# Kernel optimization log

Hardware: AMD Instinct MI355X
Metric: run time of the kernel (lower is better)

## Reference

```python
import jax, jax.numpy as jnp
import numpy as np

B, C, H, W = 8, 512, 64, 64
S = 64
STD = 0.001  # torch init.normal_(weight, std=0.001)


def setup_inputs() -> dict:
    key = jax.random.key(0)
    ks = jax.random.split(key, 7)
    return {
        "queries": jax.random.normal(ks[0], (B, C, H, W), dtype=jnp.float32),
        "k": jax.random.normal(ks[1], (B, C, H, W), dtype=jnp.float32),
        "v": jax.random.normal(ks[2], (B, C, H, W), dtype=jnp.float32),
        "Wq": jax.random.normal(ks[3], (S, C), dtype=jnp.float32) * STD,
        "Wk": jax.random.normal(ks[4], (S, C), dtype=jnp.float32) * STD,
        "Wv": jax.random.normal(ks[5], (S, C), dtype=jnp.float32) * STD,
        "Wl": jax.random.normal(ks[6], (C, S), dtype=jnp.float32) * STD,
    }


def _branch(A, Bp, Cp, Wl):
    # A,Bp,Cp: [h,w,b,S] projected tensors
    m = jnp.einsum('hwbs,hwbt->hwst', A, Bp)          # [h,w,S,S]
    m = jax.nn.softmax(m, axis=1)                      # softmax over w (dim=1, as in torch)
    o = jnp.einsum('hwst,hwbt->hwsb', m, Cp)           # [h,w,S,b]
    o = o / jnp.sum(o, axis=2, keepdims=True)          # normalize over S
    o = jnp.einsum('hwsb,cs->hwbc', o, Wl)             # transpose + Linear(S->C)
    return jnp.transpose(o, (2, 3, 0, 1))              # [b,c,h,w]


def reference(queries, k, v, Wq, Wk, Wv, Wl):
    q = jnp.transpose(queries, (2, 3, 0, 1))  # [h,w,b,c]
    kk = jnp.transpose(k, (2, 3, 0, 1))
    vv = jnp.transpose(v, (2, 3, 0, 1))
    aq = jnp.einsum('hwbc,sc->hwbs', q, Wq)   # [h,w,b,S]
    ak = jnp.einsum('hwbc,sc->hwbs', kk, Wk)
    av = jnp.einsum('hwbc,sc->hwbs', vv, Wv)
    out_q = _branch(aq, ak, av, Wl)
    out_k = _branch(ak, av, aq, Wl)
    out_v = _branch(av, aq, ak, Wl)
    return jnp.concatenate((out_q, out_k, out_v), axis=0)  # [3b,c,h,w]
```

## Files before the change

### kernel.cpp

```cpp
#include <hip/hip_runtime.h>
#include <hip/hip_bf16.h>

#define HW 4096
#define CCH 512
#define SDIM 64
#define BDIM 8

typedef __attribute__((ext_vector_type(8))) short short8;
typedef __attribute__((ext_vector_type(4))) float f32x4;

static __device__ __forceinline__ ushort f2bf(float f) {
  __hip_bfloat16 h = __float2bfloat16(f);
  return *reinterpret_cast<ushort*>(&h);
}
static __device__ __forceinline__ float bf2f(ushort u) {
  union { unsigned int u32; float f; } c;
  c.u32 = ((unsigned int)u) << 16;
  return c.f;
}
static __device__ __forceinline__ ushort trunc_bf(float f, float* rem) {
  union { float f; unsigned int u; } a; a.f = f;
  union { float f; unsigned int u; } h; h.u = a.u & 0xFFFF0000u;
  *rem = f - h.f;
  return (ushort)(a.u >> 16);
}
static __device__ __forceinline__ ushort rne_bf(float f) {
  union { float f; unsigned int u; } a; a.f = f;
  return (ushort)((a.u + 0x8000u) >> 16);
}
static __device__ __forceinline__ void gll16(const void* g, void* lds_base) {
  __builtin_amdgcn_global_load_lds(
      (const __attribute__((address_space(1))) unsigned int*)g,
      (__attribute__((address_space(3))) unsigned int*)lds_base, 16, 0, 0);
}

__global__ __launch_bounds__(256) void prep_kernel(const float* __restrict__ Wq,
                                                   const float* __restrict__ Wk,
                                                   const float* __restrict__ Wv,
                                                   const float* __restrict__ Wl,
                                                   ushort* __restrict__ whi,
                                                   ushort* __restrict__ wmid,
                                                   ushort* __restrict__ wlo,
                                                   ushort* __restrict__ wlhi,
                                                   ushort* __restrict__ wllo) {
  const int idx = blockIdx.x * 1024 + threadIdx.x * 4;
  if (blockIdx.y == 3) {
    float4 f = *reinterpret_cast<const float4*>(&Wl[idx]);
    ushort4 h, l;
    float r;
    h.x = trunc_bf(f.x, &r); l.x = rne_bf(r);
    h.y = trunc_bf(f.y, &r); l.y = rne_bf(r);
    h.z = trunc_bf(f.z, &r); l.z = rne_bf(r);
    h.w = trunc_bf(f.w, &r); l.w = rne_bf(r);
    *reinterpret_cast<ushort4*>(&wlhi[idx]) = h;
    *reinterpret_cast<ushort4*>(&wllo[idx]) = l;
    return;
  }
  const float* W = blockIdx.y == 0 ? Wq : (blockIdx.y == 1 ? Wk : Wv);
  float4 f = *reinterpret_cast<const float4*>(&W[idx]);
  ushort4 h, m, l;
  float r, r2;
  h.x = f2bf(f.x); r = f.x - bf2f(h.x); m.x = f2bf(r); r2 = r - bf2f(m.x); l.x = f2bf(r2);
  h.y = f2bf(f.y); r = f.y - bf2f(h.y); m.y = f2bf(r); r2 = r - bf2f(m.y); l.y = f2bf(r2);
  h.z = f2bf(f.z); r = f.z - bf2f(h.z); m.z = f2bf(r); r2 = r - bf2f(m.z); l.z = f2bf(r2);
  h.w = f2bf(f.w); r = f.w - bf2f(h.w); m.w = f2bf(r); r2 = r - bf2f(m.w); l.w = f2bf(r2);
  const size_t o = (size_t)blockIdx.y * (SDIM * CCH) + idx;
  *reinterpret_cast<ushort4*>(&whi[o])  = h;
  *reinterpret_cast<ushort4*>(&wmid[o]) = m;
  *reinterpret_cast<ushort4*>(&wlo[o])  = l;
}

__global__ __launch_bounds__(256) void proj_mfma_kernel(const float* __restrict__ q,
                                                        const float* __restrict__ k,
                                                        const float* __restrict__ v,
                                                        const ushort* __restrict__ whi,
                                                        const ushort* __restrict__ wmid,
                                                        const ushort* __restrict__ wlo,
                                                        float* __restrict__ ap) {
  __shared__ float Xs[2][32 * 128];
  __shared__ ushort Ws[2][3][64 * 32];
  const int mt = blockIdx.x;
  const int b = blockIdx.y;
  const int br = blockIdx.z;
  const float* x = br == 0 ? q : (br == 1 ? k : v);
  const ushort* wsrc[3] = {whi + (size_t)br * SDIM * CCH,
                           wmid + (size_t)br * SDIM * CCH,
                           wlo + (size_t)br * SDIM * CCH};
  float* apo = ap + (size_t)br * HW * 512;
  const int hw0 = mt * 128;
  const int tid = threadIdx.x;
  const int l = tid & 63;
  const int wid = tid >> 6;
  const int wstrip = wid * 32;
  const int row16 = l & 15;
  const int kgrp = l >> 4;
  const float* xcol = x + (size_t)b * CCH * HW + hw0;
  const int rbase = 8 * wid;
  const int rsub = l >> 5;
  const int wrow = wid * 16 + (l >> 2);
  const int wblk = (l & 3) ^ ((l >> 3) & 3);
  const int jp = kgrp ^ ((row16 >> 1) & 3);
  const int xswz = (kgrp & 1) << 4;

  f32x4 acc_hi[2][4] = {};
  f32x4 acc_co[2][4] = {};

#define STAGE(BUF, CI)                                                            \
  do {                                                                            \
    _Pragma("unroll") for (int j = 0; j < 4; ++j) {                               \
      const int r = rbase + 2 * j + rsub;                                         \
      const int hwsrc = (((l & 31) ^ ((((r) >> 3) & 1) << 2)) * 4);               \
      gll16(xcol + (size_t)((CI) * 32 + r) * HW + hwsrc,                          \
            &Xs[BUF][(rbase + 2 * j) * 128]);                                     \
    }                                                                             \
    _Pragma("unroll") for (int lv = 0; lv < 3; ++lv)                              \
      gll16(wsrc[lv] + (size_t)wrow * CCH + (CI) * 32 + wblk * 8,                 \
            &Ws[BUF][lv][wid * 512]);                                             \
  } while (0)

  STAGE(0, 0);

  for (int ci = 0; ci < 16; ++ci) {
    __builtin_amdgcn_sched_barrier(0);
    if (ci < 15) {
      STAGE((ci + 1) & 1, ci + 1);
      __builtin_amdgcn_sched_barrier(0);
      asm volatile("s_waitcnt vmcnt(7)" ::: "memory");
    } else {
      asm volatile("s_waitcnt vmcnt(0)" ::: "memory");
    }
    __builtin_amdgcn_sched_barrier(0);
    __builtin_amdgcn_s_barrier();
    __builtin_amdgcn_sched_barrier(0);

    short8 bh[4], bm[4], bl[4];
#pragma unroll
    for (int nf = 0; nf < 4; ++nf) {
      const int woff = (nf * 16 + row16) * 32 + jp * 8;
      bh[nf] = *reinterpret_cast<const short8*>(&Ws[ci & 1][0][woff]);
      bm[nf] = *reinterpret_cast<const short8*>(&Ws[ci & 1][1][woff]);
      bl[nf] = *reinterpret_cast<const short8*>(&Ws[ci & 1][2][woff]);
    }

    const float* lw = &Xs[ci & 1][0];
#pragma unroll
    for (int mf = 0; mf < 2; ++mf) {
      const int rowA = (wstrip + mf * 16 + row16) ^ xswz;
      short8 ah, am, al;
      {
        ushort th[8], tm[8], tl[8];
#pragma unroll
        for (int i = 0; i < 8; ++i) {
          const float f = lw[(kgrp * 8 + i) * 128 + rowA];
          float r, r2;
          th[i] = trunc_bf(f, &r);
          tm[i] = trunc_bf(r, &r2);
          tl[i] = rne_bf(r2);
        }
        ah = *reinterpret_cast<const short8*>(th);
        am = *reinterpret_cast<const short8*>(tm);
        al = *reinterpret_cast<const short8*>(tl);
      }
#pragma unroll
      for (int nf = 0; nf < 4; ++nf) {
        acc_hi[mf][nf] = __builtin_amdgcn_mfma_f32_16x16x32_bf16(ah, bh[nf], acc_hi[mf][nf], 0, 0, 0);
        acc_co[mf][nf] = __builtin_amdgcn_mfma_f32_16x16x32_bf16(ah, bm[nf], acc_co[mf][nf], 0, 0, 0);
        acc_co[mf][nf] = __builtin_amdgcn_mfma_f32_16x16x32_bf16(am, bh[nf], acc_co[mf][nf], 0, 0, 0);
        acc_co[mf][nf] = __builtin_amdgcn_mfma_f32_16x16x32_bf16(am, bm[nf], acc_co[mf][nf], 0, 0, 0);
        acc_co[mf][nf] = __builtin_amdgcn_mfma_f32_16x16x32_bf16(ah, bl[nf], acc_co[mf][nf], 0, 0, 0);
        acc_co[mf][nf] = __builtin_amdgcn_mfma_f32_16x16x32_bf16(al, bh[nf], acc_co[mf][nf], 0, 0, 0);
        acc_co[mf][nf] = __builtin_amdgcn_mfma_f32_16x16x32_bf16(am, bl[nf], acc_co[mf][nf], 0, 0, 0);
        acc_co[mf][nf] = __builtin_amdgcn_mfma_f32_16x16x32_bf16(al, bm[nf], acc_co[mf][nf], 0, 0, 0);
      }
    }
    __builtin_amdgcn_sched_barrier(0);
    __builtin_amdgcn_s_barrier();
    __builtin_amdgcn_sched_barrier(0);
  }
#undef STAGE

#pragma unroll
  for (int mf = 0; mf < 2; ++mf)
#pragma unroll
    for (int nf = 0; nf < 4; ++nf)
#pragma unroll
      for (int r = 0; r < 4; ++r) {
        const int m = hw0 + wstrip + mf * 16 + kgrp * 4 + r;
        apo[(size_t)m * 512 + b * 64 + nf * 16 + row16] = acc_hi[mf][nf][r] + acc_co[mf][nf][r];
      }
}

__global__ __launch_bounds__(512) void denom_kernel(const float* __restrict__ ap,
                                                    float* __restrict__ rD) {
  __shared__ float As[3][128];
  __shared__ float Bs[3][512];
  const int h = blockIdx.x, br = blockIdx.y, sq = blockIdx.z;
  const float* A  = ap + ((size_t)br * HW + (size_t)h * 64) * 512;
  const float* Bp = ap + ((size_t)((br + 1) % 3) * HW + (size_t)h * 64) * 512;
  const int tid = threadIdx.x;
  const int t = tid & 63;
  const int sg = tid >> 6;
  float D[2] = {};

#define STAGE_D(BUF, W)                                                        \
  do {                                                                         \
    if (sg == 0) {                                                             \
      if (t < 32)                                                              \
        gll16(A + (size_t)(W) * 512 + (t >> 2) * 64 + sq * 16 + (t & 3) * 4,   \
              &As[BUF][0]);                                                    \
    } else if (sg == 1) {                                                      \
      gll16(Bp + (size_t)(W) * 512 + t * 4, &Bs[BUF][0]);                      \
    } else if (sg == 2) {                                                      \
      gll16(Bp + (size_t)(W) * 512 + 256 + t * 4, &Bs[BUF][256]);              \
    }                                                                          \
  } while (0)

  STAGE_D(0, 0);

  for (int w = 0; w < 64; ++w) {
    __builtin_amdgcn_sched_barrier(0);
    if (w < 63) {
      STAGE_D((w + 1) % 3, w + 1);
      __builtin_amdgcn_sched_barrier(0);
      asm volatile("s_waitcnt vmcnt(1)" ::: "memory");
    } else {
      asm volatile("s_waitcnt vmcnt(0)" ::: "memory");
    }
    __builtin_amdgcn_sched_barrier(0);
    __builtin_amdgcn_s_barrier();
    __builtin_amdgcn_sched_barrier(0);

    const float* Aw = &As[w % 3][0];
    const float* Bw = &Bs[w % 3][0];
    float bv[8];
#pragma unroll
    for (int b = 0; b < 8; ++b) bv[b] = Bw[b * 64 + t];
#pragma unroll
    for (int j = 0; j < 2; ++j) {
      const int sl = sg * 2 + j;
      float m = 0.f;
#pragma unroll
      for (int b = 0; b < 8; ++b) m = fmaf(Aw[b * 16 + sl], bv[b], m);
      D[j] += __expf(m);
    }
  }
#undef STAGE_D

#pragma unroll
  for (int j = 0; j < 2; ++j)
    rD[((size_t)(br * 64 + h) * 64 + sq * 16 + sg * 2 + j) * 64 + t] = 1.0f / D[j];
}

__global__ __launch_bounds__(256) void attn_kernel(const float* __restrict__ ap,
                                                   const float* __restrict__ rD,
                                                   float* __restrict__ on) {
  __shared__ float Tile[3][3 * 512];
  __shared__ float Ms[64 * 68];
  const int wc = blockIdx.x, h = blockIdx.y, br = blockIdx.z;
  const float* A  = ap + ((size_t)br * HW + h * 64) * 512;
  const float* Bp = ap + ((size_t)((br + 1) % 3) * HW + h * 64) * 512;
  const float* Cp = ap + ((size_t)((br + 2) % 3) * HW + h * 64) * 512;
  const float* rDp = rD + (size_t)(br * 64 + h) * 4096;
  const int tid = threadIdx.x;
  const int t = tid & 63;
  const int sg = tid >> 6;
  const int w0 = wc * 8;

  float rdv[16];
#pragma unroll
  for (int j = 0; j < 16; ++j) rdv[j] = rDp[(sg * 16 + j) * 64 + t];

  const float* src = sg == 0 ? A : (sg == 1 ? Bp : Cp);

#define STAGE_T(BUF, W)                                                   \
  do {                                                                    \
    if (sg < 3) {                                                         \
      _Pragma("unroll") for (int j = 0; j < 2; ++j)                       \
        gll16(src + (size_t)(W) * 512 + j * 256 + t * 4,                  \
              &Tile[BUF][sg * 512 + j * 256]);                            \
    }                                                                     \
  } while (0)

  STAGE_T(0, w0);

  for (int wi = 0; wi < 8; ++wi) {
    __builtin_amdgcn_sched_barrier(0);
    if (wi < 7) {
      STAGE_T((wi + 1) % 3, w0 + wi + 1);
      __builtin_amdgcn_sched_barrier(0);
      asm volatile("s_waitcnt vmcnt(2)" ::: "memory");
    } else {
      asm volatile("s_waitcnt vmcnt(0)" ::: "memory");
    }
    __builtin_amdgcn_sched_barrier(0);
    asm volatile("s_waitcnt lgkmcnt(0)" ::: "memory");
    __builtin_amdgcn_s_barrier();
    __builtin_amdgcn_sched_barrier(0);

    const float* Aw = &Tile[wi % 3][0];
    const float* Bw = &Tile[wi % 3][512];
    const float* Cw = &Tile[wi % 3][1024];
    {
      float bv[8];
#pragma unroll
      for (int b = 0; b < 8; ++b) bv[b] = Bw[b * 64 + t];
#pragma unroll
      for (int j4 = 0; j4 < 4; ++j4) {
        const int s0 = sg * 16 + j4 * 4;
        float4 ma = make_float4(0.f, 0.f, 0.f, 0.f);
#pragma unroll
        for (int b = 0; b < 8; ++b) {
          const float4 av = *reinterpret_cast<const float4*>(&Aw[b * 64 + s0]);
          ma.x = fmaf(av.x, bv[b], ma.x);
          ma.y = fmaf(av.y, bv[b], ma.y);
          ma.z = fmaf(av.z, bv[b], ma.z);
          ma.w = fmaf(av.w, bv[b], ma.w);
        }
        Ms[(s0 + 0) * 68 + t] = __expf(ma.x) * rdv[j4 * 4 + 0];
        Ms[(s0 + 1) * 68 + t] = __expf(ma.y) * rdv[j4 * 4 + 1];
        Ms[(s0 + 2) * 68 + t] = __expf(ma.z) * rdv[j4 * 4 + 2];
        Ms[(s0 + 3) * 68 + t] = __expf(ma.w) * rdv[j4 * 4 + 3];
      }
    }
    __builtin_amdgcn_sched_barrier(0);
    asm volatile("s_waitcnt lgkmcnt(0)" ::: "memory");
    __builtin_amdgcn_s_barrier();
    __builtin_amdgcn_sched_barrier(0);

    float o0 = 0.f, o1 = 0.f;
#pragma unroll
    for (int tt = 0; tt < 64; tt += 4) {
      const float4 mv = *reinterpret_cast<const float4*>(&Ms[t * 68 + tt]);
      const float4 c0 = *reinterpret_cast<const float4*>(&Cw[sg * 64 + tt]);
      const float4 c1 = *reinterpret_cast<const float4*>(&Cw[(sg + 4) * 64 + tt]);
      o0 = fmaf(mv.w, c0.w, fmaf(mv.z, c0.z, fmaf(mv.y, c0.y, fmaf(mv.x, c0.x, o0))));
      o1 = fmaf(mv.w, c1.w, fmaf(mv.z, c1.z, fmaf(mv.y, c1.y, fmaf(mv.x, c1.x, o1))));
    }
    float n0 = o0, n1 = o1;
#pragma unroll
    for (int off = 32; off > 0; off >>= 1) {
      n0 += __shfl_xor(n0, off);
      n1 += __shfl_xor(n1, off);
    }
    const float r0 = 1.0f / n0, r1 = 1.0f / n1;
    const size_t ob = ((size_t)br * HW + h * 64 + w0 + wi) * 512;
    on[ob + (size_t)sg * 64 + t] = o0 * r0;
    on[ob + (size_t)(sg + 4) * 64 + t] = o1 * r1;
  }
#undef STAGE_T
}

__global__ __launch_bounds__(256) void out_kernel(const float* __restrict__ on,
                                                  const ushort* __restrict__ wlhi,
                                                  const ushort* __restrict__ wllo,
                                                  float* __restrict__ out) {
  __shared__ float Os[128 * 68];
  const int hwt = blockIdx.x;
  const int brb = blockIdx.y;
  const int br = brb >> 3, b = brb & 7;
  const int hw0 = hwt * 128;
  const int tid = threadIdx.x;
  const int l = tid & 63;
  const int wv = tid >> 6;
  const int l15 = l & 15;
  const int kgrp = l >> 4;

  {
    const int row = tid >> 4;
    const int s4 = (tid & 15) * 4;
#pragma unroll
    for (int it = 0; it < 8; ++it) {
      const int r = row + it * 16;
      *reinterpret_cast<float4*>(&Os[r * 68 + s4]) =
          *reinterpret_cast<const float4*>(&on[((size_t)(br * HW + hw0 + r) * 8 + b) * 64 + s4]);
    }
  }
  __syncthreads();

  short8 onh[2][2], onl[2][2];
#pragma unroll
  for (int nf = 0; nf < 2; ++nf)
#pragma unroll
    for (int ks = 0; ks < 2; ++ks) {
      const int row = wv * 32 + nf * 16 + l15;
      const float* p = &Os[row * 68 + ks * 32 + kgrp * 8];
      ushort th[8], tl[8];
#pragma unroll
      for (int i = 0; i < 8; ++i) {
        float r;
        th[i] = trunc_bf(p[i], &r);
        tl[i] = rne_bf(r);
      }
      onh[nf][ks] = *reinterpret_cast<const short8*>(th);
      onl[nf][ks] = *reinterpret_cast<const short8*>(tl);
    }

  for (int mf = 0; mf < 32; ++mf) {
    f32x4 acc[2] = {};
#pragma unroll
    for (int ks = 0; ks < 2; ++ks) {
      const size_t woff = (size_t)(mf * 16 + l15) * 64 + ks * 32 + kgrp * 8;
      const short8 wh8 = *reinterpret_cast<const short8*>(&wlhi[woff]);
      const short8 wl8 = *reinterpret_cast<const short8*>(&wllo[woff]);
#pragma unroll
      for (int nf = 0; nf < 2; ++nf) {
        acc[nf] = __builtin_amdgcn_mfma_f32_16x16x32_bf16(wh8, onh[nf][ks], acc[nf], 0, 0, 0);
        acc[nf] = __builtin_amdgcn_mfma_f32_16x16x32_bf16(wh8, onl[nf][ks], acc[nf], 0, 0, 0);
        acc[nf] = __builtin_amdgcn_mfma_f32_16x16x32_bf16(wl8, onh[nf][ks], acc[nf], 0, 0, 0);
      }
    }
#pragma unroll
    for (int nf = 0; nf < 2; ++nf)
#pragma unroll
      for (int r = 0; r < 4; ++r) {
        const int cc = mf * 16 + kgrp * 4 + r;
        out[(size_t)(brb * 512 + cc) * HW + hw0 + wv * 32 + nf * 16 + l15] = acc[nf][r];
      }
  }
}

extern "C" void kernel_launch(void* const* d_in, const int* in_sizes, int n_in,
                              void* d_out, int out_size, void* d_ws, size_t ws_size,
                              hipStream_t stream) {
  const float* q  = (const float*)d_in[0];
  const float* k  = (const float*)d_in[1];
  const float* v  = (const float*)d_in[2];
  const float* Wq = (const float*)d_in[3];
  const float* Wk = (const float*)d_in[4];
  const float* Wv = (const float*)d_in[5];
  const float* Wl = (const float*)d_in[6];
  float* out = (float*)d_out;

  float* ap = (float*)d_ws;
  float* rD = ap + (size_t)3 * HW * 512;
  float* on = rD + (size_t)3 * 64 * 64 * 64;
  ushort* whi  = (ushort*)rD;
  ushort* wmid = whi + (size_t)3 * SDIM * CCH;
  ushort* wlo  = wmid + (size_t)3 * SDIM * CCH;
  ushort* wlhi = (ushort*)(on + (size_t)3 * HW * 512);
  ushort* wllo = wlhi + (size_t)SDIM * CCH;

  prep_kernel<<<dim3(32, 4), 256, 0, stream>>>(Wq, Wk, Wv, Wl, whi, wmid, wlo, wlhi, wllo);
  proj_mfma_kernel<<<dim3(32, 8, 3), 256, 0, stream>>>(q, k, v, whi, wmid, wlo, ap);
  denom_kernel<<<dim3(64, 3, 4), 512, 0, stream>>>(ap, rD);
  attn_kernel<<<dim3(8, 64, 3), 256, 0, stream>>>(ap, rD, on);
  out_kernel<<<dim3(32, 24), 256, 0, stream>>>(on, wlhi, wllo, out);
}
```

Measured before the change: 234.7 us.

## Software-pipeline attn_kernel: overlap PV of previous column with QK of next

Double-buffers the Ms score tile in shared memory so that each iteration computes the PV product for column wi-1 and the QK/exp scores for column wi between a single barrier. This cuts the per-column barrier count from two to one and lets the two phases interleave. In exchange it doubles Ms shared memory, which may lower occupancy. It also waits on vmcnt(0) instead of keeping one prefetch in flight.

```diff
diff --git a/kernel.cpp b/kernel.cpp
--- a/kernel.cpp
+++ b/kernel.cpp
@@ -255,7 +255,7 @@
                                                    const float* __restrict__ rD,
                                                    float* __restrict__ on) {
   __shared__ float Tile[3][3 * 512];
-  __shared__ float Ms[64 * 68];
+  __shared__ float Ms[2][64 * 68];
   const int wc = blockIdx.x, h = blockIdx.y, br = blockIdx.z;
   const float* A  = ap + ((size_t)br * HW + h * 64) * 512;
   const float* Bp = ap + ((size_t)((br + 1) % 3) * HW + h * 64) * 512;
@@ -281,73 +281,78 @@
     }                                                                     \
   } while (0)
 
+#define QK(MB, TB)                                                        \
+  do {                                                                    \
+    const float* Aw = &Tile[TB][0];                                       \
+    const float* Bw = &Tile[TB][512];                                     \
+    float bv[8];                                                          \
+    _Pragma("unroll") for (int b = 0; b < 8; ++b) bv[b] = Bw[b * 64 + t]; \
+    _Pragma("unroll") for (int j4 = 0; j4 < 4; ++j4) {                    \
+      const int s0 = sg * 16 + j4 * 4;                                    \
+      float4 ma = make_float4(0.f, 0.f, 0.f, 0.f);                        \
+      _Pragma("unroll") for (int b = 0; b < 8; ++b) {                     \
+        const float4 av = *reinterpret_cast<const float4*>(&Aw[b * 64 + s0]); \
+        ma.x = fmaf(av.x, bv[b], ma.x);                                   \
+        ma.y = fmaf(av.y, bv[b], ma.y);                                   \
+        ma.z = fmaf(av.z, bv[b], ma.z);                                   \
+        ma.w = fmaf(av.w, bv[b], ma.w);                                   \
+      }                                                                   \
+      Ms[MB][(s0 + 0) * 68 + t] = __expf(ma.x) * rdv[j4 * 4 + 0];         \
+      Ms[MB][(s0 + 1) * 68 + t] = __expf(ma.y) * rdv[j4 * 4 + 1];         \
+      Ms[MB][(s0 + 2) * 68 + t] = __expf(ma.z) * rdv[j4 * 4 + 2];         \
+      Ms[MB][(s0 + 3) * 68 + t] = __expf(ma.w) * rdv[j4 * 4 + 3];         \
+    }                                                                     \
+  } while (0)
+
+#define PV(MB, TB, WIDX)                                                  \
+  do {                                                                    \
+    const float* Cw = &Tile[TB][1024];                                    \
+    float o0 = 0.f, o1 = 0.f;                                             \
+    _Pragma("unroll") for (int tt = 0; tt < 64; tt += 4) {                \
+      const float4 mv = *reinterpret_cast<const float4*>(&Ms[MB][t * 68 + tt]); \
+      const float4 c0 = *reinterpret_cast<const float4*>(&Cw[sg * 64 + tt]);    \
+      const float4 c1 = *reinterpret_cast<const float4*>(&Cw[(sg + 4) * 64 + tt]); \
+      o0 = fmaf(mv.w, c0.w, fmaf(mv.z, c0.z, fmaf(mv.y, c0.y, fmaf(mv.x, c0.x, o0)))); \
+      o1 = fmaf(mv.w, c1.w, fmaf(mv.z, c1.z, fmaf(mv.y, c1.y, fmaf(mv.x, c1.x, o1)))); \
+    }                                                                     \
+    float n0 = o0, n1 = o1;                                               \
+    _Pragma("unroll") for (int off = 32; off > 0; off >>= 1) {            \
+      n0 += __shfl_xor(n0, off);                                          \
+      n1 += __shfl_xor(n1, off);                                          \
+    }                                                                     \
+    const float r0 = 1.0f / n0, r1 = 1.0f / n1;                           \
+    const size_t ob = ((size_t)br * HW + h * 64 + (WIDX)) * 512;          \
+    on[ob + (size_t)sg * 64 + t] = o0 * r0;                               \
+    on[ob + (size_t)(sg + 4) * 64 + t] = o1 * r1;                         \
+  } while (0)
+
   STAGE_T(0, w0);
-
-  for (int wi = 0; wi < 8; ++wi) {
-    __builtin_amdgcn_sched_barrier(0);
-    if (wi < 7) {
-      STAGE_T((wi + 1) % 3, w0 + wi + 1);
-      __builtin_amdgcn_sched_barrier(0);
-      asm volatile("s_waitcnt vmcnt(2)" ::: "memory");
-    } else {
-      asm volatile("s_waitcnt vmcnt(0)" ::: "memory");
-    }
+  asm volatile("s_waitcnt vmcnt(0)" ::: "memory");
+  __builtin_amdgcn_s_barrier();
+  __builtin_amdgcn_sched_barrier(0);
+  STAGE_T(1, w0 + 1);
+  QK(0, 0);
+
+  for (int wi = 1; wi < 8; ++wi) {
+    __builtin_amdgcn_sched_barrier(0);
+    asm volatile("s_waitcnt vmcnt(0)" ::: "memory");
     __builtin_amdgcn_sched_barrier(0);
     asm volatile("s_waitcnt lgkmcnt(0)" ::: "memory");
     __builtin_amdgcn_s_barrier();
     __builtin_amdgcn_sched_barrier(0);
-
-    const float* Aw = &Tile[wi % 3][0];
-    const float* Bw = &Tile[wi % 3][512];
-    const float* Cw = &Tile[wi % 3][1024];
-    {
-      float bv[8];
-#pragma unroll
-      for (int b = 0; b < 8; ++b) bv[b] = Bw[b * 64 + t];
-#pragma unroll
-      for (int j4 = 0; j4 < 4; ++j4) {
-        const int s0 = sg * 16 + j4 * 4;
-        float4 ma = make_float4(0.f, 0.f, 0.f, 0.f);
-#pragma unroll
-        for (int b = 0; b < 8; ++b) {
-          const float4 av = *reinterpret_cast<const float4*>(&Aw[b * 64 + s0]);
-          ma.x = fmaf(av.x, bv[b], ma.x);
-          ma.y = fmaf(av.y, bv[b], ma.y);
-          ma.z = fmaf(av.z, bv[b], ma.z);
-          ma.w = fmaf(av.w, bv[b], ma.w);
-        }
-        Ms[(s0 + 0) * 68 + t] = __expf(ma.x) * rdv[j4 * 4 + 0];
-        Ms[(s0 + 1) * 68 + t] = __expf(ma.y) * rdv[j4 * 4 + 1];
-        Ms[(s0 + 2) * 68 + t] = __expf(ma.z) * rdv[j4 * 4 + 2];
-        Ms[(s0 + 3) * 68 + t] = __expf(ma.w) * rdv[j4 * 4 + 3];
-      }
-    }
-    __builtin_amdgcn_sched_barrier(0);
-    asm volatile("s_waitcnt lgkmcnt(0)" ::: "memory");
-    __builtin_amdgcn_s_barrier();
-    __builtin_amdgcn_sched_barrier(0);
-
-    float o0 = 0.f, o1 = 0.f;
-#pragma unroll
-    for (int tt = 0; tt < 64; tt += 4) {
-      const float4 mv = *reinterpret_cast<const float4*>(&Ms[t * 68 + tt]);
-      const float4 c0 = *reinterpret_cast<const float4*>(&Cw[sg * 64 + tt]);
-      const float4 c1 = *reinterpret_cast<const float4*>(&Cw[(sg + 4) * 64 + tt]);
-      o0 = fmaf(mv.w, c0.w, fmaf(mv.z, c0.z, fmaf(mv.y, c0.y, fmaf(mv.x, c0.x, o0))));
-      o1 = fmaf(mv.w, c1.w, fmaf(mv.z, c1.z, fmaf(mv.y, c1.y, fmaf(mv.x, c1.x, o1))));
-    }
-    float n0 = o0, n1 = o1;
-#pragma unroll
-    for (int off = 32; off > 0; off >>= 1) {
-      n0 += __shfl_xor(n0, off);
-      n1 += __shfl_xor(n1, off);
-    }
-    const float r0 = 1.0f / n0, r1 = 1.0f / n1;
-    const size_t ob = ((size_t)br * HW + h * 64 + w0 + wi) * 512;
-    on[ob + (size_t)sg * 64 + t] = o0 * r0;
-    on[ob + (size_t)(sg + 4) * 64 + t] = o1 * r1;
-  }
+    if (wi < 7) STAGE_T((wi + 1) % 3, w0 + wi + 1);
+    __builtin_amdgcn_sched_barrier(0);
+    PV((wi - 1) & 1, (wi - 1) % 3, w0 + wi - 1);
+    QK(wi & 1, wi % 3);
+  }
+  __builtin_amdgcn_sched_barrier(0);
+  asm volatile("s_waitcnt lgkmcnt(0)" ::: "memory");
+  __builtin_amdgcn_s_barrier();
+  __builtin_amdgcn_sched_barrier(0);
+  PV(7 & 1, 7 % 3, w0 + 7);
 #undef STAGE_T
+#undef QK
+#undef PV
 }
 
 __global__ __launch_bounds__(256) void out_kernel(const float* __restrict__ on,
```

After: 236.7 us. About the same (+0.9%).
